# Kernel optimization log

Measured on AMD Instinct MI355X. Metric: run time of the kernel, lower is better.

The kernel has to match this reference:

```python
import jax, jax.numpy as jnp
import numpy as np
from jax import lax

B, T, I = 8192, 784, 1
H, C = 30, 10


def setup_inputs() -> dict:
    key = jax.random.key(0)
    ks = jax.random.split(key, 6)
    inputs = jax.random.normal(ks[0], (B, T, I), dtype=jnp.float32)
    # RNN cell params (expRNN-style modReLU cell): input kernel (no bias),
    # recurrent kernel (no bias), modReLU bias.
    W_ih = jax.random.normal(ks[1], (H, I), dtype=jnp.float32) / np.sqrt(I)
    W_hh = jax.random.normal(ks[2], (H, H), dtype=jnp.float32) / np.sqrt(H)
    b_mod = jax.random.normal(ks[3], (H,), dtype=jnp.float32) * 0.01
    # Final classifier Linear(hidden_size, num_classes)
    W_lin = jax.random.normal(ks[4], (C, H), dtype=jnp.float32) / np.sqrt(H)
    b_lin = jax.random.normal(ks[5], (C,), dtype=jnp.float32) * 0.01
    return {"inputs": inputs, "W_ih": W_ih, "W_hh": W_hh, "b_mod": b_mod,
            "W_lin": W_lin, "b_lin": b_lin}


def _modrelu(z, b):
    # modReLU: sign(z) * relu(|z| + b)
    return jnp.sign(z) * jax.nn.relu(jnp.abs(z) + b)


def reference(inputs, W_ih, W_hh, b_mod, W_lin, b_lin):
    # inputs: [B, T, 1]; recurrence over T with hidden state [B, H]
    xs = jnp.swapaxes(inputs, 0, 1)  # [T, B, I]

    def step(h, x_t):
        z = x_t @ W_ih.T + h @ W_hh.T  # [B, H]
        h_new = _modrelu(z, b_mod)
        return h_new, None

    h0 = jnp.zeros((inputs.shape[0], W_hh.shape[0]), dtype=inputs.dtype)
    h_final, _ = lax.scan(step, h0, xs)
    return h_final @ W_lin.T + b_lin  # [B, C] logits
```

## Files before the change

### kernel.cpp

```cpp
#include <hip/hip_runtime.h>


#define T_STEPS 784
#define NBATCH  8192
#define NH      30
#define NC      10
#define BPB     8
#define XPAD    788

typedef float v2f __attribute__((ext_vector_type(2)));

#define ROR2(dst, src, S) \
    dst = __int_as_float(__builtin_amdgcn_update_dpp( \
        0, __float_as_int(src), 0x120 + 2*(S), 0xf, 0xf, true))

#define PIN8(a,b,c,d,e,f,g,h) \
    asm volatile("" : "+v"(a),"+v"(b),"+v"(c),"+v"(d), \
                      "+v"(e),"+v"(f),"+v"(g),"+v"(h))

__global__ __launch_bounds__(64, 1)
void rnn_modrelu_l8(const float* __restrict__ inp,
                    const float* __restrict__ W_ih,
                    const float* __restrict__ W_hh,
                    const float* __restrict__ b_mod,
                    const float* __restrict__ W_lin,
                    const float* __restrict__ b_lin,
                    float* __restrict__ out)
{
    __shared__ __align__(16) float xl[BPB * XPAD];
    __shared__ __align__(16) float wl[NH * NH];
    __shared__ float hfin[BPB * 32];

    const int l     = threadIdx.x;
    const int blk   = blockIdx.x;
    const int w16   = l & 15;
    const int row16 = l >> 4;
    const int u     = w16 >> 1;
    const int bl    = 2 * row16 + (w16 & 1);

    {
        const float4* src = (const float4*)(inp + (size_t)blk * (BPB * T_STEPS));
        #pragma unroll
        for (int k = 0; k < 25; ++k) {
            int v = l + 64 * k;
            if (v < (BPB * T_STEPS) / 4) {
                int b   = v / 196;
                int rem = v - b * 196;
                *(float4*)(xl + b * XPAD + 4 * rem) = src[v];
            }
        }
    }
    {
        const float4* src = (const float4*)W_hh;
        #pragma unroll
        for (int k = 0; k < 4; ++k) {
            int idx = l + 64 * k;
            if (idx < (NH * NH) / 4) ((float4*)wl)[idx] = src[idx];
        }
    }
    __syncthreads();

    const int r0 = 4 * u;
    float wq[8][4][4];
    #pragma unroll
    for (int s = 0; s < 8; ++s) {
        const int c = (u - s) & 7;
        #pragma unroll
        for (int r = 0; r < 4; ++r) {
            const int row = r0 + r;
            #pragma unroll
            for (int j = 0; j < 4; ++j) {
                const int col = 4 * c + j;
                wq[s][r][j] = (row < NH && col < NH) ? wl[row * NH + col] : 0.0f;
            }
        }
    }
    float wih[4], bm[4];
    #pragma unroll
    for (int r = 0; r < 4; ++r) {
        const int row = r0 + r;
        wih[r] = (row < NH) ? W_ih[row]  : 0.0f;
        bm[r]  = (row < NH) ? b_mod[row] : 0.0f;
    }
    #pragma unroll
    for (int s = 0; s < 8; ++s) {
        PIN8(wq[s][0][0], wq[s][0][1], wq[s][0][2], wq[s][0][3],
             wq[s][1][0], wq[s][1][1], wq[s][1][2], wq[s][1][3]);
        PIN8(wq[s][2][0], wq[s][2][1], wq[s][2][2], wq[s][2][3],
             wq[s][3][0], wq[s][3][1], wq[s][3][2], wq[s][3][3]);
    }

    const float* xb = xl + bl * XPAD;
    float xcur = xb[0];
    float h0 = 0.0f, h1 = 0.0f, h2 = 0.0f, h3 = 0.0f;

    #pragma unroll 1
    for (int t = 0; t < T_STEPS; ++t) {
        int tn = t + 1; if (tn >= T_STEPS) tn = T_STEPS - 1;
        const float xnext = xb[tn];

        float z0 = wih[0] * xcur;
        float z1 = wih[1] * xcur;
        float z2 = wih[2] * xcur;
        float z3 = wih[3] * xcur;

        #pragma unroll
        for (int j = 0; j < 4; ++j) {
            const float q = (j == 0) ? h0 : (j == 1) ? h1 : (j == 2) ? h2 : h3;
            z0 = fmaf(wq[0][0][j], q, z0);
            z1 = fmaf(wq[0][1][j], q, z1);
            z2 = fmaf(wq[0][2][j], q, z2);
            z3 = fmaf(wq[0][3][j], q, z3);
        }

#define SSTEP(S) { \
        float q0, q1, q2, q3; \
        ROR2(q0, h0, S); ROR2(q1, h1, S); ROR2(q2, h2, S); ROR2(q3, h3, S); \
        z0 = fmaf(wq[S][0][0], q0, z0); z1 = fmaf(wq[S][1][0], q0, z1); \
        z2 = fmaf(wq[S][2][0], q0, z2); z3 = fmaf(wq[S][3][0], q0, z3); \
        z0 = fmaf(wq[S][0][1], q1, z0); z1 = fmaf(wq[S][1][1], q1, z1); \
        z2 = fmaf(wq[S][2][1], q1, z2); z3 = fmaf(wq[S][3][1], q1, z3); \
        z0 = fmaf(wq[S][0][2], q2, z0); z1 = fmaf(wq[S][1][2], q2, z1); \
        z2 = fmaf(wq[S][2][2], q2, z2); z3 = fmaf(wq[S][3][2], q2, z3); \
        z0 = fmaf(wq[S][0][3], q3, z0); z1 = fmaf(wq[S][1][3], q3, z1); \
        z2 = fmaf(wq[S][2][3], q3, z2); z3 = fmaf(wq[S][3][3], q3, z3); \
}
        SSTEP(1) SSTEP(2) SSTEP(3) SSTEP(4) SSTEP(5) SSTEP(6) SSTEP(7)
#undef SSTEP

        h0 = copysignf(fmaxf(fabsf(z0) + bm[0], 0.0f), z0);
        h1 = copysignf(fmaxf(fabsf(z1) + bm[1], 0.0f), z1);
        h2 = copysignf(fmaxf(fabsf(z2) + bm[2], 0.0f), z2);
        h3 = copysignf(fmaxf(fabsf(z3) + bm[3], 0.0f), z3);

        xcur = xnext;
    }

    hfin[bl * 32 + r0 + 0] = h0;
    hfin[bl * 32 + r0 + 1] = h1;
    hfin[bl * 32 + r0 + 2] = h2;
    hfin[bl * 32 + r0 + 3] = h3;
    __syncthreads();

    #pragma unroll
    for (int it = 0; it < 2; ++it) {
        const int k = l + 64 * it;
        if (k < BPB * NC) {
            const int bbo = k / NC;
            const int c   = k % NC;
            float acc = b_lin[c];
            #pragma unroll
            for (int i = 0; i < NH; ++i) {
                acc = fmaf(W_lin[c * NH + i], hfin[bbo * 32 + i], acc);
            }
            out[((size_t)blk * BPB + bbo) * NC + c] = acc;
        }
    }
}

extern "C" void kernel_launch(void* const* d_in, const int* in_sizes, int n_in,
                              void* d_out, int out_size, void* d_ws, size_t ws_size,
                              hipStream_t stream) {
    const float* inp   = (const float*)d_in[0];
    const float* W_ih  = (const float*)d_in[1];
    const float* W_hh  = (const float*)d_in[2];
    const float* b_mod = (const float*)d_in[3];
    const float* W_lin = (const float*)d_in[4];
    const float* b_lin = (const float*)d_in[5];
    float* out = (float*)d_out;

    dim3 grid(NBATCH / BPB);
    dim3 block(64);
    rnn_modrelu_l8<<<grid, block, 0, stream>>>(inp, W_ih, W_hh, b_mod,
                                               W_lin, b_lin, out);
}
```

Before: 250.9 us.

## Run recurrent matvec on MFMA using split-bf16 emulation of fp32

Replaces the per-lane FMA and DPP-rotation recurrence with 32x32x16 bf16 MFMA instructions. Each wavefront now handles 32 batch rows instead of 8, so the grid shrinks to 256 blocks. W_hh and the hidden state are split into three bf16 terms to approximate fp32 accuracy, and six cross products per half are accumulated. The new hidden state is redistributed between lane halves with permlane32 swaps. This adds per-step conversion and pack work and relies on the three-term split to stay accurate over 784 steps. The smaller grid may leave many compute units idle.

```diff
diff --git a/kernel.cpp b/kernel.cpp
--- a/kernel.cpp
+++ b/kernel.cpp
@@ -5,156 +5,202 @@
 #define NBATCH  8192
 #define NH      30
 #define NC      10
-#define BPB     8
+#define BPW     32
 #define XPAD    788
 
-typedef float v2f __attribute__((ext_vector_type(2)));
-
-#define ROR2(dst, src, S) \
-    dst = __int_as_float(__builtin_amdgcn_update_dpp( \
-        0, __float_as_int(src), 0x120 + 2*(S), 0xf, 0xf, true))
-
-#define PIN8(a,b,c,d,e,f,g,h) \
-    asm volatile("" : "+v"(a),"+v"(b),"+v"(c),"+v"(d), \
-                      "+v"(e),"+v"(f),"+v"(g),"+v"(h))
+typedef float  f32x16 __attribute__((ext_vector_type(16)));
+typedef short  s16x8  __attribute__((ext_vector_type(8)));
+typedef int    i32x4  __attribute__((ext_vector_type(4)));
+
+#define MFMA32(a, b, c) __builtin_amdgcn_mfma_f32_32x32x16_bf16(a, b, c, 0, 0, 0)
+
+__device__ __forceinline__ int cvt_pk_bf16(float lo, float hi) {
+    int d;
+    asm("v_cvt_pk_bf16_f32 %0, %1, %2" : "=v"(d) : "v"(lo), "v"(hi));
+    return d;
+}
+
+__device__ __forceinline__ void permswap(int &x, int &y) {
+#if __has_builtin(__builtin_amdgcn_permlane32_swap)
+    auto rr = __builtin_amdgcn_permlane32_swap(x, y, false, false);
+    int t0, t1;
+    __builtin_memcpy(&t0, (const char*)&rr, 4);
+    __builtin_memcpy(&t1, (const char*)&rr + 4, 4);
+    x = t0; y = t1;
+#else
+    asm volatile("s_nop 1\n\tv_permlane32_swap_b32 %0, %1\n\ts_nop 1"
+                 : "+v"(x), "+v"(y));
+#endif
+}
+
+__device__ __forceinline__ float rne_bf16(float x) {
+    unsigned u = __float_as_uint(x);
+    u = (u + 0x7fffu + ((u >> 16) & 1u)) & 0xffff0000u;
+    return __uint_as_float(u);
+}
+
+__device__ __forceinline__ s16x8 pack8(const float* v) {
+    i32x4 t;
+    t.x = cvt_pk_bf16(v[0], v[1]);
+    t.y = cvt_pk_bf16(v[2], v[3]);
+    t.z = cvt_pk_bf16(v[4], v[5]);
+    t.w = cvt_pk_bf16(v[6], v[7]);
+    return __builtin_bit_cast(s16x8, t);
+}
 
 __global__ __launch_bounds__(64, 1)
-void rnn_modrelu_l8(const float* __restrict__ inp,
-                    const float* __restrict__ W_ih,
-                    const float* __restrict__ W_hh,
-                    const float* __restrict__ b_mod,
-                    const float* __restrict__ W_lin,
-                    const float* __restrict__ b_lin,
-                    float* __restrict__ out)
+void rnn_mfma(const float* __restrict__ inp,
+              const float* __restrict__ W_ih,
+              const float* __restrict__ W_hh,
+              const float* __restrict__ b_mod,
+              const float* __restrict__ W_lin,
+              const float* __restrict__ b_lin,
+              float* __restrict__ out)
 {
-    __shared__ __align__(16) float xl[BPB * XPAD];
-    __shared__ __align__(16) float wl[NH * NH];
-    __shared__ float hfin[BPB * 32];
-
-    const int l     = threadIdx.x;
-    const int blk   = blockIdx.x;
-    const int w16   = l & 15;
-    const int row16 = l >> 4;
-    const int u     = w16 >> 1;
-    const int bl    = 2 * row16 + (w16 & 1);
+    __shared__ __align__(16) float xl[BPW * XPAD];
+    __shared__ float hfin[BPW * 33];
+
+    const int l   = threadIdx.x;
+    const int blk = blockIdx.x;
+    const int b   = l & 31;
+    const int sg  = l >> 5;
 
     {
-        const float4* src = (const float4*)(inp + (size_t)blk * (BPB * T_STEPS));
-        #pragma unroll
-        for (int k = 0; k < 25; ++k) {
-            int v = l + 64 * k;
-            if (v < (BPB * T_STEPS) / 4) {
-                int b   = v / 196;
-                int rem = v - b * 196;
-                *(float4*)(xl + b * XPAD + 4 * rem) = src[v];
+        const float4* src = (const float4*)(inp + (size_t)blk * (BPW * T_STEPS));
+        #pragma unroll 1
+        for (int k = 0; k < 98; ++k) {
+            int v   = l + 64 * k;
+            int bb  = v / 196;
+            int rem = v - bb * 196;
+            *(float4*)(xl + bb * XPAD + 4 * rem) = src[v];
+        }
+    }
+    __syncthreads();
+
+    s16x8 wA[3][2];
+    {
+        #pragma unroll
+        for (int c = 0; c < 2; ++c) {
+            float w1f[8], w2f[8], w3f[8];
+            #pragma unroll
+            for (int e = 0; e < 8; ++e) {
+                int k = 16 * c + 8 * sg + e;
+                float w  = (b < NH && k < NH) ? W_hh[b * NH + k] : 0.0f;
+                float a1 = rne_bf16(w);  float r1 = w  - a1;
+                float a2 = rne_bf16(r1); float r2 = r1 - a2;
+                float a3 = rne_bf16(r2);
+                w1f[e] = a1; w2f[e] = a2; w3f[e] = a3;
             }
-        }
-    }
+            wA[0][c] = pack8(w1f);
+            wA[1][c] = pack8(w2f);
+            wA[2][c] = pack8(w3f);
+        }
+    }
+
+    float wihr[16], bmr[16];
+    #pragma unroll
+    for (int j = 0; j < 16; ++j) {
+        int r = (j & 3) + 8 * (j >> 2) + 4 * sg;
+        wihr[j] = (r < NH) ? W_ih[r]  : 0.0f;
+        bmr[j]  = (r < NH) ? b_mod[r] : 0.0f;
+    }
+
+    f32x16 czero;
+    #pragma unroll
+    for (int j = 0; j < 16; ++j) czero[j] = 0.0f;
+
+    s16x8 fB[3][2];
     {
-        const float4* src = (const float4*)W_hh;
-        #pragma unroll
-        for (int k = 0; k < 4; ++k) {
-            int idx = l + 64 * k;
-            if (idx < (NH * NH) / 4) ((float4*)wl)[idx] = src[idx];
-        }
-    }
-    __syncthreads();
-
-    const int r0 = 4 * u;
-    float wq[8][4][4];
-    #pragma unroll
-    for (int s = 0; s < 8; ++s) {
-        const int c = (u - s) & 7;
-        #pragma unroll
-        for (int r = 0; r < 4; ++r) {
-            const int row = r0 + r;
-            #pragma unroll
-            for (int j = 0; j < 4; ++j) {
-                const int col = 4 * c + j;
-                wq[s][r][j] = (row < NH && col < NH) ? wl[row * NH + col] : 0.0f;
-            }
-        }
-    }
-    float wih[4], bm[4];
-    #pragma unroll
-    for (int r = 0; r < 4; ++r) {
-        const int row = r0 + r;
-        wih[r] = (row < NH) ? W_ih[row]  : 0.0f;
-        bm[r]  = (row < NH) ? b_mod[row] : 0.0f;
-    }
-    #pragma unroll
-    for (int s = 0; s < 8; ++s) {
-        PIN8(wq[s][0][0], wq[s][0][1], wq[s][0][2], wq[s][0][3],
-             wq[s][1][0], wq[s][1][1], wq[s][1][2], wq[s][1][3]);
-        PIN8(wq[s][2][0], wq[s][2][1], wq[s][2][2], wq[s][2][3],
-             wq[s][3][0], wq[s][3][1], wq[s][3][2], wq[s][3][3]);
-    }
-
-    const float* xb = xl + bl * XPAD;
+        i32x4 zi = {0, 0, 0, 0};
+        s16x8 z8 = __builtin_bit_cast(s16x8, zi);
+        #pragma unroll
+        for (int lv = 0; lv < 3; ++lv) { fB[lv][0] = z8; fB[lv][1] = z8; }
+    }
+
+    float hq[16];
+    const float* xb = xl + b * XPAD;
     float xcur = xb[0];
-    float h0 = 0.0f, h1 = 0.0f, h2 = 0.0f, h3 = 0.0f;
 
     #pragma unroll 1
     for (int t = 0; t < T_STEPS; ++t) {
-        int tn = t + 1; if (tn >= T_STEPS) tn = T_STEPS - 1;
-        const float xnext = xb[tn];
-
-        float z0 = wih[0] * xcur;
-        float z1 = wih[1] * xcur;
-        float z2 = wih[2] * xcur;
-        float z3 = wih[3] * xcur;
-
-        #pragma unroll
-        for (int j = 0; j < 4; ++j) {
-            const float q = (j == 0) ? h0 : (j == 1) ? h1 : (j == 2) ? h2 : h3;
-            z0 = fmaf(wq[0][0][j], q, z0);
-            z1 = fmaf(wq[0][1][j], q, z1);
-            z2 = fmaf(wq[0][2][j], q, z2);
-            z3 = fmaf(wq[0][3][j], q, z3);
-        }
-
-#define SSTEP(S) { \
-        float q0, q1, q2, q3; \
-        ROR2(q0, h0, S); ROR2(q1, h1, S); ROR2(q2, h2, S); ROR2(q3, h3, S); \
-        z0 = fmaf(wq[S][0][0], q0, z0); z1 = fmaf(wq[S][1][0], q0, z1); \
-        z2 = fmaf(wq[S][2][0], q0, z2); z3 = fmaf(wq[S][3][0], q0, z3); \
-        z0 = fmaf(wq[S][0][1], q1, z0); z1 = fmaf(wq[S][1][1], q1, z1); \
-        z2 = fmaf(wq[S][2][1], q1, z2); z3 = fmaf(wq[S][3][1], q1, z3); \
-        z0 = fmaf(wq[S][0][2], q2, z0); z1 = fmaf(wq[S][1][2], q2, z1); \
-        z2 = fmaf(wq[S][2][2], q2, z2); z3 = fmaf(wq[S][3][2], q2, z3); \
-        z0 = fmaf(wq[S][0][3], q3, z0); z1 = fmaf(wq[S][1][3], q3, z1); \
-        z2 = fmaf(wq[S][2][3], q3, z2); z3 = fmaf(wq[S][3][3], q3, z3); \
-}
-        SSTEP(1) SSTEP(2) SSTEP(3) SSTEP(4) SSTEP(5) SSTEP(6) SSTEP(7)
-#undef SSTEP
-
-        h0 = copysignf(fmaxf(fabsf(z0) + bm[0], 0.0f), z0);
-        h1 = copysignf(fmaxf(fabsf(z1) + bm[1], 0.0f), z1);
-        h2 = copysignf(fmaxf(fabsf(z2) + bm[2], 0.0f), z2);
-        h3 = copysignf(fmaxf(fabsf(z3) + bm[3], 0.0f), z3);
+        float xnext = xb[t + 1];
+
+        f32x16 cA;
+        #pragma unroll
+        for (int j = 0; j < 16; ++j) cA[j] = wihr[j] * xcur;
+
+        f32x16 accA, accB;
+        accA = MFMA32(wA[0][0], fB[0][0], cA);
+        accB = MFMA32(wA[0][1], fB[0][1], czero);
+        accA = MFMA32(wA[0][0], fB[1][0], accA);
+        accB = MFMA32(wA[0][1], fB[1][1], accB);
+        accA = MFMA32(wA[1][0], fB[0][0], accA);
+        accB = MFMA32(wA[1][1], fB[0][1], accB);
+        accA = MFMA32(wA[0][0], fB[2][0], accA);
+        accB = MFMA32(wA[0][1], fB[2][1], accB);
+        accA = MFMA32(wA[1][0], fB[1][0], accA);
+        accB = MFMA32(wA[1][1], fB[1][1], accB);
+        accA = MFMA32(wA[2][0], fB[0][0], accA);
+        accB = MFMA32(wA[2][1], fB[0][1], accB);
+
+        #pragma unroll
+        for (int j = 0; j < 16; ++j) {
+            float z = accA[j] + accB[j];
+            float m = fmaxf(fabsf(z) + bmr[j], 0.0f);
+            hq[j] = copysignf(m, z);
+        }
+
+        int P1[8], P2[8], P3[8];
+        #pragma unroll
+        for (int q = 0; q < 8; ++q) {
+            float a = hq[2 * q], c = hq[2 * q + 1];
+            int p1 = cvt_pk_bf16(a, c);
+            float ua = __uint_as_float(((unsigned)p1) << 16);
+            float uc = __uint_as_float(((unsigned)p1) & 0xffff0000u);
+            float ra = a - ua, rc = c - uc;
+            int p2 = cvt_pk_bf16(ra, rc);
+            float va = __uint_as_float(((unsigned)p2) << 16);
+            float vc = __uint_as_float(((unsigned)p2) & 0xffff0000u);
+            int p3 = cvt_pk_bf16(ra - va, rc - vc);
+            P1[q] = p1; P2[q] = p2; P3[q] = p3;
+        }
+
+#define SWAPBUILD(P, lv) { \
+        int a0 = P[0], a1 = P[1], a2 = P[2], a3 = P[3]; \
+        int a4 = P[4], a5 = P[5], a6 = P[6], a7 = P[7]; \
+        permswap(a0, a2); permswap(a1, a3); \
+        permswap(a4, a6); permswap(a5, a7); \
+        i32x4 t0 = {a0, a1, a2, a3}; \
+        i32x4 t1 = {a4, a5, a6, a7}; \
+        fB[lv][0] = __builtin_bit_cast(s16x8, t0); \
+        fB[lv][1] = __builtin_bit_cast(s16x8, t1); \
+}
+        SWAPBUILD(P1, 0)
+        SWAPBUILD(P2, 1)
+        SWAPBUILD(P3, 2)
+#undef SWAPBUILD
 
         xcur = xnext;
     }
 
-    hfin[bl * 32 + r0 + 0] = h0;
-    hfin[bl * 32 + r0 + 1] = h1;
-    hfin[bl * 32 + r0 + 2] = h2;
-    hfin[bl * 32 + r0 + 3] = h3;
+    #pragma unroll
+    for (int j = 0; j < 16; ++j) {
+        int r = (j & 3) + 8 * (j >> 2) + 4 * sg;
+        hfin[b * 33 + r] = hq[j];
+    }
     __syncthreads();
 
     #pragma unroll
-    for (int it = 0; it < 2; ++it) {
-        const int k = l + 64 * it;
-        if (k < BPB * NC) {
-            const int bbo = k / NC;
-            const int c   = k % NC;
-            float acc = b_lin[c];
-            #pragma unroll
-            for (int i = 0; i < NH; ++i) {
-                acc = fmaf(W_lin[c * NH + i], hfin[bbo * 32 + i], acc);
-            }
-            out[((size_t)blk * BPB + bbo) * NC + c] = acc;
-        }
+    for (int it = 0; it < 5; ++it) {
+        int kk = l + 64 * it;
+        int bb = kk / 10;
+        int c  = kk - bb * 10;
+        float acc = b_lin[c];
+        #pragma unroll
+        for (int i = 0; i < NH; ++i) {
+            acc = fmaf(W_lin[c * NH + i], hfin[bb * 33 + i], acc);
+        }
+        out[((size_t)blk * BPW + bb) * NC + c] = acc;
     }
 }
 
@@ -169,8 +215,8 @@
     const float* b_lin = (const float*)d_in[5];
     float* out = (float*)d_out;
 
-    dim3 grid(NBATCH / BPB);
+    dim3 grid(NBATCH / BPW);
     dim3 block(64);
-    rnn_modrelu_l8<<<grid, block, 0, stream>>>(inp, W_ih, W_hh, b_mod,
-                                               W_lin, b_lin, out);
-}
+    rnn_mfma<<<grid, block, 0, stream>>>(inp, W_ih, W_hh, b_mod,
+                                         W_lin, b_lin, out);
+}
```

Measured after the change: 555.8 us. 122% more time.
